# Optimization experiments

Measured on AMD Instinct MI355X. Metric: run time of the kernel, lower is better.

## Reference

```python
import jax, jax.numpy as jnp
import numpy as np

T, B, IN, H1, H2, OUT = 1024, 512, 20, 128, 64, 3

def _uniform(key, shape, bound):
    return jax.random.uniform(key, shape, jnp.float32, -bound, bound)

def setup_inputs() -> dict:
    key = jax.random.key(0)
    ks = jax.random.split(key, 11)
    b1 = 1.0 / np.sqrt(H1)
    b2 = 1.0 / np.sqrt(H2)
    return {
        "x": jax.random.normal(ks[0], (T, B, IN), jnp.float32),
        "W_ih0": _uniform(ks[1], (4 * H1, IN), b1),
        "W_hh0": _uniform(ks[2], (4 * H1, H1), b1),
        "b_ih0": _uniform(ks[3], (4 * H1,), b1),
        "b_hh0": _uniform(ks[4], (4 * H1,), b1),
        "W_ih1": _uniform(ks[5], (4 * H2, H1), b2),
        "W_hh1": _uniform(ks[6], (4 * H2, H2), b2),
        "b_ih1": _uniform(ks[7], (4 * H2,), b2),
        "b_hh1": _uniform(ks[8], (4 * H2,), b2),
        "W_d": _uniform(ks[9], (OUT, H2), b2),
        "b_d": _uniform(ks[10], (OUT,), b2),
    }

def _lstm_layer(x, W_ih, W_hh, b_ih, b_hh, hidden):
    # x: (T, B, in_dim); PyTorch gate order: i, f, g, o
    batch = x.shape[1]
    x_proj = jnp.einsum("tbi,gi->tbg", x, W_ih) + (b_ih + b_hh)  # (T,B,4H)

    def step(carry, xp):
        h, c = carry
        gates = xp + h @ W_hh.T  # (B,4H)
        i, f, g, o = jnp.split(gates, 4, axis=-1)
        i = jax.nn.sigmoid(i)
        f = jax.nn.sigmoid(f)
        g = jnp.tanh(g)
        o = jax.nn.sigmoid(o)
        c = f * c + i * g
        h = o * jnp.tanh(c)
        return (h, c), h

    h0 = jnp.zeros((batch, hidden), x.dtype)
    c0 = jnp.zeros((batch, hidden), x.dtype)
    _, ys = jax.lax.scan(step, (h0, c0), x_proj)
    return ys  # (T, B, H)

def reference(x, W_ih0, W_hh0, b_ih0, b_hh0, W_ih1, W_hh1, b_ih1, b_hh1, W_d, b_d):
    h1 = _lstm_layer(x, W_ih0, W_hh0, b_ih0, b_hh0, H1)   # (T,B,128)
    h2 = _lstm_layer(h1, W_ih1, W_hh1, b_ih1, b_hh1, H2)  # (T,B,64)
    # Faithful to original: lstm_out[:, -1, :] in seq-first layout picks the
    # last batch element at every timestep -> (T, 64)
    last = h2[:, -1, :]
    act = jax.nn.relu(last)
    # Dropout in eval mode is identity.
    return act @ W_d.T + b_d  # (T, 3)
```

## Files before the change

kernel.cpp:

```cpp
#include <hip/hip_runtime.h>
#include <hip/hip_bf16.h>


#define T_STEPS 1024
#define BATCH   512
#define IN_F    20
#define H1_     128
#define H2_     64
#define OUT_F   3
#define G1_     (4*H1_)
#define G2_     (4*H2_)

typedef float f4 __attribute__((ext_vector_type(4)));
typedef unsigned int u32;
typedef u32 u4 __attribute__((ext_vector_type(4)));
typedef _Float16 h2 __attribute__((ext_vector_type(2)));

__device__ __forceinline__ float sigmoidf_(float x) {
    return 1.0f / (1.0f + __expf(-x));
}
__device__ __forceinline__ float tanhf_(float x) {
    return 1.0f - 2.0f / (__expf(2.0f * x) + 1.0f);
}
__device__ __forceinline__ h2 as_h2(u32 v) {
    union { u32 u; h2 h; } c; c.u = v; return c.h;
}
__device__ __forceinline__ u32 pkh(float a, float b) {
    union { _Float16 h[2]; u32 u; } c;
    c.h[0] = (_Float16)a; c.h[1] = (_Float16)b; return c.u;
}
__device__ __forceinline__ float fdot2_(h2 a, h2 b, float c) {
#if __has_builtin(__builtin_amdgcn_fdot2)
    return __builtin_amdgcn_fdot2(a, b, c, false);
#else
    float d = c;
    asm("v_dot2_f32_f16 %0, %1, %2, %0" : "+v"(d) : "v"(a), "v"(b));
    return d;
#endif
}

__global__ void xproj_kernel(const float* __restrict__ x,
                             const float* __restrict__ W_ih0,
                             const float* __restrict__ b_ih0,
                             const float* __restrict__ b_hh0,
                             float* __restrict__ xp1)
{
    const int t = blockIdx.x;
    const int g = threadIdx.x;
    const float* xr = x + ((size_t)t * BATCH + (BATCH - 1)) * IN_F;
    const float* w  = W_ih0 + g * IN_F;
    float acc = b_ih0[g] + b_hh0[g];
#pragma unroll
    for (int i = 0; i < IN_F; ++i) acc = fmaf(xr[i], w[i], acc);
    xp1[t * G1_ + g] = acc;
}

__global__ __attribute__((amdgpu_flat_work_group_size(512, 512),
                          amdgpu_waves_per_eu(2, 2)))
void lstm1_kernel(const float* __restrict__ xp1,
                  const float* __restrict__ W_hh0,
                  float* __restrict__ h1seq)
{
    const int tid = threadIdx.x;

    __shared__ u4    swW[512 * 17];
    __shared__ u4    shhi[16];
    __shared__ u4    shlo[16];
    __shared__ float sg[G1_];

    {
        const float* wr = W_hh0 + (size_t)tid * H1_;
#pragma unroll
        for (int j = 0; j < 16; ++j) {
            const f4 lo = *(const f4*)(wr + j * 8);
            const f4 hi = *(const f4*)(wr + j * 8 + 4);
            u4 pk;
            pk.x = pkh(lo.x, lo.y);
            pk.y = pkh(lo.z, lo.w);
            pk.z = pkh(hi.x, hi.y);
            pk.w = pkh(hi.z, hi.w);
            swW[tid * 17 + j] = pk;
        }
    }
    if (tid < 16) { shhi[tid] = u4{0,0,0,0}; shlo[tid] = u4{0,0,0,0}; }
    float c1 = 0.0f;
    __syncthreads();

    const u4* wrow = swW + tid * 17;
    float xp_cur = xp1[tid];

    for (int t = 0; t < T_STEPS; ++t) {
        float xp_next;
        {
            const int tn = (t + 1 < T_STEPS) ? (t + 1) : (T_STEPS - 1);
            xp_next = xp1[(size_t)tn * G1_ + tid];
        }

        float a0 = 0.f, a1 = 0.f, a2 = 0.f, a3 = 0.f;
#pragma unroll
        for (int j = 0; j < 16; ++j) {
            const u4 wq = wrow[j];
            const u4 hh = shhi[j];
            const u4 hl = shlo[j];
            a0 = fdot2_(as_h2(wq.x), as_h2(hh.x), a0);
            a1 = fdot2_(as_h2(wq.y), as_h2(hh.y), a1);
            a0 = fdot2_(as_h2(wq.z), as_h2(hh.z), a0);
            a1 = fdot2_(as_h2(wq.w), as_h2(hh.w), a1);
            a2 = fdot2_(as_h2(wq.x), as_h2(hl.x), a2);
            a3 = fdot2_(as_h2(wq.y), as_h2(hl.y), a3);
            a2 = fdot2_(as_h2(wq.z), as_h2(hl.z), a2);
            a3 = fdot2_(as_h2(wq.w), as_h2(hl.w), a3);
        }
        sg[tid] = ((a0 + a1) + 0.000244140625f * (a2 + a3)) + xp_cur;
        __syncthreads();

        if (tid < H1_) {
            const float vi = sg[tid];
            const float vf = sg[H1_ + tid];
            const float vg = sg[2 * H1_ + tid];
            const float vo = sg[3 * H1_ + tid];
            c1 = fmaf(sigmoidf_(vf), c1, sigmoidf_(vi) * tanhf_(vg));
            const float h = sigmoidf_(vo) * tanhf_(c1);
            const _Float16 hh16 = (_Float16)h;
            const float hrem = (h - (float)hh16) * 4096.0f;
            ((_Float16*)shhi)[tid] = hh16;
            ((_Float16*)shlo)[tid] = (_Float16)hrem;
            h1seq[(size_t)t * H1_ + tid] = h;
        }
        __syncthreads();
        xp_cur = xp_next;
    }
}

__global__ void xproj2_kernel(const float* __restrict__ h1seq,
                              const float* __restrict__ W_ih1,
                              const float* __restrict__ b_ih1,
                              const float* __restrict__ b_hh1,
                              float* __restrict__ xp2)
{
    const int t = blockIdx.x;
    const int g = threadIdx.x;
    __shared__ f4 sh[H1_ / 4];
    if (g < H1_ / 4) sh[g] = ((const f4*)(h1seq + (size_t)t * H1_))[g];
    __syncthreads();
    const f4* w = (const f4*)(W_ih1 + (size_t)g * H1_);
    float ax = 0.f, ay = 0.f, az = 0.f, aw = 0.f;
#pragma unroll
    for (int k = 0; k < H1_ / 4; ++k) {
        const f4 h4 = sh[k]; const f4 w4 = w[k];
        ax = fmaf(w4.x, h4.x, ax); ay = fmaf(w4.y, h4.y, ay);
        az = fmaf(w4.z, h4.z, az); aw = fmaf(w4.w, h4.w, aw);
    }
    xp2[(size_t)t * G2_ + g] = ((ax + ay) + (az + aw)) + b_ih1[g] + b_hh1[g];
}

__global__ __attribute__((amdgpu_flat_work_group_size(256, 256),
                          amdgpu_waves_per_eu(1, 1)))
void lstm2_kernel(const float* __restrict__ xp2,
                  const float* __restrict__ W_hh1,
                  float* __restrict__ h2seq)
{
    const int tid = threadIdx.x;

    __shared__ u4    swW2[256 * 9];
    __shared__ u4    shhi[8];
    __shared__ u4    shlo[8];
    __shared__ float sg2[G2_];

    {
        const float* wr = W_hh1 + (size_t)tid * H2_;
#pragma unroll
        for (int j = 0; j < 8; ++j) {
            const f4 lo = *(const f4*)(wr + j * 8);
            const f4 hi = *(const f4*)(wr + j * 8 + 4);
            u4 pk;
            pk.x = pkh(lo.x, lo.y);
            pk.y = pkh(lo.z, lo.w);
            pk.z = pkh(hi.x, hi.y);
            pk.w = pkh(hi.z, hi.w);
            swW2[tid * 9 + j] = pk;
        }
    }
    if (tid < 8) { shhi[tid] = u4{0,0,0,0}; shlo[tid] = u4{0,0,0,0}; }
    float c2 = 0.0f;
    __syncthreads();

    const u4* wrow = swW2 + tid * 9;
    float xp_cur = xp2[tid];

    for (int t = 0; t < T_STEPS; ++t) {
        float xp_next;
        {
            const int tn = (t + 1 < T_STEPS) ? (t + 1) : (T_STEPS - 1);
            xp_next = xp2[(size_t)tn * G2_ + tid];
        }

        float a0 = 0.f, a1 = 0.f, a2 = 0.f, a3 = 0.f;
#pragma unroll
        for (int j = 0; j < 8; ++j) {
            const u4 wq = wrow[j];
            const u4 hh = shhi[j];
            const u4 hl = shlo[j];
            a0 = fdot2_(as_h2(wq.x), as_h2(hh.x), a0);
            a1 = fdot2_(as_h2(wq.y), as_h2(hh.y), a1);
            a0 = fdot2_(as_h2(wq.z), as_h2(hh.z), a0);
            a1 = fdot2_(as_h2(wq.w), as_h2(hh.w), a1);
            a2 = fdot2_(as_h2(wq.x), as_h2(hl.x), a2);
            a3 = fdot2_(as_h2(wq.y), as_h2(hl.y), a3);
            a2 = fdot2_(as_h2(wq.z), as_h2(hl.z), a2);
            a3 = fdot2_(as_h2(wq.w), as_h2(hl.w), a3);
        }
        sg2[tid] = ((a0 + a1) + 0.000244140625f * (a2 + a3)) + xp_cur;
        __syncthreads();

        if (tid < H2_) {
            const float vi = sg2[tid];
            const float vf = sg2[H2_ + tid];
            const float vg = sg2[2 * H2_ + tid];
            const float vo = sg2[3 * H2_ + tid];
            c2 = fmaf(sigmoidf_(vf), c2, sigmoidf_(vi) * tanhf_(vg));
            const float h = sigmoidf_(vo) * tanhf_(c2);
            const _Float16 hh16 = (_Float16)h;
            const float hrem = (h - (float)hh16) * 4096.0f;
            ((_Float16*)shhi)[tid] = hh16;
            ((_Float16*)shlo)[tid] = (_Float16)hrem;
            h2seq[(size_t)t * H2_ + tid] = h;
        }
        __syncthreads();
        xp_cur = xp_next;
    }
}

__global__ void head_kernel(const float* __restrict__ h2seq,
                            const float* __restrict__ W_d,
                            const float* __restrict__ b_d,
                            float* __restrict__ out)
{
    const int idx = blockIdx.x * blockDim.x + threadIdx.x;
    if (idx >= T_STEPS * OUT_F) return;
    const int t = idx / OUT_F;
    const int o = idx - t * OUT_F;
    const float* hr = h2seq + (size_t)t * H2_;
    const float* w  = W_d + o * H2_;
    float acc = b_d[o];
#pragma unroll
    for (int j = 0; j < H2_; ++j) acc = fmaf(fmaxf(hr[j], 0.0f), w[j], acc);
    out[idx] = acc;
}

extern "C" void kernel_launch(void* const* d_in, const int* in_sizes, int n_in,
                              void* d_out, int out_size, void* d_ws, size_t ws_size,
                              hipStream_t stream) {
    const float* x     = (const float*)d_in[0];
    const float* W_ih0 = (const float*)d_in[1];
    const float* W_hh0 = (const float*)d_in[2];
    const float* b_ih0 = (const float*)d_in[3];
    const float* b_hh0 = (const float*)d_in[4];
    const float* W_ih1 = (const float*)d_in[5];
    const float* W_hh1 = (const float*)d_in[6];
    const float* b_ih1 = (const float*)d_in[7];
    const float* b_hh1 = (const float*)d_in[8];
    const float* W_d   = (const float*)d_in[9];
    const float* b_d   = (const float*)d_in[10];

    float* out   = (float*)d_out;
    float* xp1   = (float*)d_ws;
    float* h1seq = xp1 + (size_t)T_STEPS * G1_;
    float* h2seq = h1seq + (size_t)T_STEPS * H1_;
    float* xp2   = xp1;

    hipLaunchKernelGGL(xproj_kernel, dim3(T_STEPS), dim3(G1_), 0, stream,
                       x, W_ih0, b_ih0, b_hh0, xp1);
    hipLaunchKernelGGL(lstm1_kernel, dim3(1), dim3(512), 0, stream,
                       xp1, W_hh0, h1seq);
    hipLaunchKernelGGL(xproj2_kernel, dim3(T_STEPS), dim3(G2_), 0, stream,
                       h1seq, W_ih1, b_ih1, b_hh1, xp2);
    hipLaunchKernelGGL(lstm2_kernel, dim3(1), dim3(256), 0, stream,
                       xp2, W_hh1, h2seq);
    hipLaunchKernelGGL(head_kernel, dim3((T_STEPS * OUT_F + 255) / 256), dim3(256),
                       0, stream, h2seq, W_d, b_d, out);
}
```

Baseline: 1.962 ms.

## Split LSTM recurrent dot products across twice the threads with split-K reduction

```diff
diff --git a/kernel.cpp b/kernel.cpp
--- a/kernel.cpp
+++ b/kernel.cpp
@@ -14,7 +14,7 @@
 typedef float f4 __attribute__((ext_vector_type(4)));
 typedef unsigned int u32;
 typedef u32 u4 __attribute__((ext_vector_type(4)));
-typedef _Float16 h2 __attribute__((ext_vector_type(2)));
+typedef _Float16 h2t __attribute__((ext_vector_type(2)));
 
 __device__ __forceinline__ float sigmoidf_(float x) {
     return 1.0f / (1.0f + __expf(-x));
@@ -22,14 +22,14 @@
 __device__ __forceinline__ float tanhf_(float x) {
     return 1.0f - 2.0f / (__expf(2.0f * x) + 1.0f);
 }
-__device__ __forceinline__ h2 as_h2(u32 v) {
-    union { u32 u; h2 h; } c; c.u = v; return c.h;
+__device__ __forceinline__ h2t as_h2(u32 v) {
+    union { u32 u; h2t h; } c; c.u = v; return c.h;
 }
 __device__ __forceinline__ u32 pkh(float a, float b) {
     union { _Float16 h[2]; u32 u; } c;
     c.h[0] = (_Float16)a; c.h[1] = (_Float16)b; return c.u;
 }
-__device__ __forceinline__ float fdot2_(h2 a, h2 b, float c) {
+__device__ __forceinline__ float fdot2_(h2t a, h2t b, float c) {
 #if __has_builtin(__builtin_amdgcn_fdot2)
     return __builtin_amdgcn_fdot2(a, b, c, false);
 #else
@@ -38,6 +38,27 @@
     return d;
 #endif
 }
+__device__ __forceinline__ u4 packq(const float* p) {
+    const f4 a = *(const f4*)p;
+    const f4 b = *(const f4*)(p + 4);
+    u4 pk;
+    pk.x = pkh(a.x, a.y); pk.y = pkh(a.z, a.w);
+    pk.z = pkh(b.x, b.y); pk.w = pkh(b.z, b.w);
+    return pk;
+}
+
+#define LO_SCALE_INV 0.000244140625f
+
+#define DOTQ(WQ, HH, HL)                                                      \
+    { const u4 hh_ = (HH); const u4 hl_ = (HL);                               \
+      a0 = fdot2_(as_h2((WQ).x), as_h2(hh_.x), a0);                           \
+      a1 = fdot2_(as_h2((WQ).y), as_h2(hh_.y), a1);                           \
+      a0 = fdot2_(as_h2((WQ).z), as_h2(hh_.z), a0);                           \
+      a1 = fdot2_(as_h2((WQ).w), as_h2(hh_.w), a1);                           \
+      a2 = fdot2_(as_h2((WQ).x), as_h2(hl_.x), a2);                           \
+      a3 = fdot2_(as_h2((WQ).y), as_h2(hl_.y), a3);                           \
+      a2 = fdot2_(as_h2((WQ).z), as_h2(hl_.z), a2);                           \
+      a3 = fdot2_(as_h2((WQ).w), as_h2(hl_.w), a3); }
 
 __global__ void xproj_kernel(const float* __restrict__ x,
                              const float* __restrict__ W_ih0,
@@ -55,70 +76,80 @@
     xp1[t * G1_ + g] = acc;
 }
 
-__global__ __attribute__((amdgpu_flat_work_group_size(512, 512),
-                          amdgpu_waves_per_eu(2, 2)))
+__global__ void pack_kernel(const float* __restrict__ W_hh0,
+                            const float* __restrict__ W_hh1,
+                            u4* __restrict__ wpk1,
+                            u4* __restrict__ wpk2)
+{
+    const int idx = blockIdx.x * blockDim.x + threadIdx.x;
+    if (idx < 4096) {
+        const int r = idx >> 2, qq = idx & 3;
+        const int g = r & 511, hf = r >> 9;
+        wpk1[r * 4 + qq] = packq(W_hh0 + (size_t)g * H1_ + hf * 64 + 32 + 8 * qq);
+    } else if (idx < 4096 + 1024) {
+        const int i2 = idx - 4096;
+        const int r2 = i2 >> 1, qq = i2 & 1;
+        const int g2 = r2 & 255, hf = r2 >> 8;
+        wpk2[r2 * 2 + qq] = packq(W_hh1 + (size_t)g2 * H2_ + hf * 32 + 16 + 8 * qq);
+    }
+}
+
+__global__ __attribute__((amdgpu_flat_work_group_size(1024, 1024),
+                          amdgpu_waves_per_eu(4, 4)))
 void lstm1_kernel(const float* __restrict__ xp1,
                   const float* __restrict__ W_hh0,
+                  const u4* __restrict__ wpk1,
                   float* __restrict__ h1seq)
 {
     const int tid = threadIdx.x;
-
-    __shared__ u4    swW[512 * 17];
+    const int g   = tid & 511;
+    const int hf  = tid >> 9;
+    const int r   = hf * 512 + g;
+
+    __shared__ u4    swW[1024 * 5];
     __shared__ u4    shhi[16];
     __shared__ u4    shlo[16];
-    __shared__ float sg[G1_];
+    __shared__ float sp1[1024];
 
     {
-        const float* wr = W_hh0 + (size_t)tid * H1_;
-#pragma unroll
-        for (int j = 0; j < 16; ++j) {
-            const f4 lo = *(const f4*)(wr + j * 8);
-            const f4 hi = *(const f4*)(wr + j * 8 + 4);
-            u4 pk;
-            pk.x = pkh(lo.x, lo.y);
-            pk.y = pkh(lo.z, lo.w);
-            pk.z = pkh(hi.x, hi.y);
-            pk.w = pkh(hi.z, hi.w);
-            swW[tid * 17 + j] = pk;
-        }
+        const float* wr = W_hh0 + (size_t)g * H1_ + hf * 64;
+#pragma unroll
+        for (int q = 0; q < 4; ++q) swW[r * 5 + q] = packq(wr + q * 8);
     }
     if (tid < 16) { shhi[tid] = u4{0,0,0,0}; shlo[tid] = u4{0,0,0,0}; }
     float c1 = 0.0f;
     __syncthreads();
 
-    const u4* wrow = swW + tid * 17;
-    float xp_cur = xp1[tid];
+    const u4* wk = wpk1 + (size_t)r * 4;
+    float xp_cur = (hf == 0) ? xp1[g] : 0.0f;
 
     for (int t = 0; t < T_STEPS; ++t) {
-        float xp_next;
-        {
+        float xp_next = 0.0f;
+        if (hf == 0) {
             const int tn = (t + 1 < T_STEPS) ? (t + 1) : (T_STEPS - 1);
-            xp_next = xp1[(size_t)tn * G1_ + tid];
-        }
+            xp_next = xp1[(size_t)tn * G1_ + g];
+        }
+        const u4 w4_ = wk[0], w5_ = wk[1], w6_ = wk[2], w7_ = wk[3];
 
         float a0 = 0.f, a1 = 0.f, a2 = 0.f, a3 = 0.f;
 #pragma unroll
-        for (int j = 0; j < 16; ++j) {
-            const u4 wq = wrow[j];
-            const u4 hh = shhi[j];
-            const u4 hl = shlo[j];
-            a0 = fdot2_(as_h2(wq.x), as_h2(hh.x), a0);
-            a1 = fdot2_(as_h2(wq.y), as_h2(hh.y), a1);
-            a0 = fdot2_(as_h2(wq.z), as_h2(hh.z), a0);
-            a1 = fdot2_(as_h2(wq.w), as_h2(hh.w), a1);
-            a2 = fdot2_(as_h2(wq.x), as_h2(hl.x), a2);
-            a3 = fdot2_(as_h2(wq.y), as_h2(hl.y), a3);
-            a2 = fdot2_(as_h2(wq.z), as_h2(hl.z), a2);
-            a3 = fdot2_(as_h2(wq.w), as_h2(hl.w), a3);
-        }
-        sg[tid] = ((a0 + a1) + 0.000244140625f * (a2 + a3)) + xp_cur;
+        for (int q = 0; q < 4; ++q) {
+            const u4 wq = swW[r * 5 + q];
+            DOTQ(wq, shhi[hf * 8 + q], shlo[hf * 8 + q]);
+        }
+        DOTQ(w4_, shhi[hf * 8 + 4], shlo[hf * 8 + 4]);
+        DOTQ(w5_, shhi[hf * 8 + 5], shlo[hf * 8 + 5]);
+        DOTQ(w6_, shhi[hf * 8 + 6], shlo[hf * 8 + 6]);
+        DOTQ(w7_, shhi[hf * 8 + 7], shlo[hf * 8 + 7]);
+
+        sp1[g * 2 + hf] = ((a0 + a1) + LO_SCALE_INV * (a2 + a3)) + xp_cur;
         __syncthreads();
 
         if (tid < H1_) {
-            const float vi = sg[tid];
-            const float vf = sg[H1_ + tid];
-            const float vg = sg[2 * H1_ + tid];
-            const float vo = sg[3 * H1_ + tid];
+            const float vi = sp1[tid * 2]              + sp1[tid * 2 + 1];
+            const float vf = sp1[(H1_ + tid) * 2]      + sp1[(H1_ + tid) * 2 + 1];
+            const float vg = sp1[(2 * H1_ + tid) * 2]  + sp1[(2 * H1_ + tid) * 2 + 1];
+            const float vo = sp1[(3 * H1_ + tid) * 2]  + sp1[(3 * H1_ + tid) * 2 + 1];
             c1 = fmaf(sigmoidf_(vf), c1, sigmoidf_(vi) * tanhf_(vg));
             const float h = sigmoidf_(vo) * tanhf_(c1);
             const _Float16 hh16 = (_Float16)h;
@@ -154,70 +185,61 @@
     xp2[(size_t)t * G2_ + g] = ((ax + ay) + (az + aw)) + b_ih1[g] + b_hh1[g];
 }
 
-__global__ __attribute__((amdgpu_flat_work_group_size(256, 256),
-                          amdgpu_waves_per_eu(1, 1)))
+__global__ __attribute__((amdgpu_flat_work_group_size(512, 512),
+                          amdgpu_waves_per_eu(2, 2)))
 void lstm2_kernel(const float* __restrict__ xp2,
                   const float* __restrict__ W_hh1,
+                  const u4* __restrict__ wpk2,
                   float* __restrict__ h2seq)
 {
     const int tid = threadIdx.x;
-
-    __shared__ u4    swW2[256 * 9];
+    const int g2  = tid & 255;
+    const int hf  = tid >> 8;
+    const int r2  = hf * 256 + g2;
+
+    __shared__ u4    swW2[512 * 3];
     __shared__ u4    shhi[8];
     __shared__ u4    shlo[8];
-    __shared__ float sg2[G2_];
+    __shared__ float sp2[512];
 
     {
-        const float* wr = W_hh1 + (size_t)tid * H2_;
-#pragma unroll
-        for (int j = 0; j < 8; ++j) {
-            const f4 lo = *(const f4*)(wr + j * 8);
-            const f4 hi = *(const f4*)(wr + j * 8 + 4);
-            u4 pk;
-            pk.x = pkh(lo.x, lo.y);
-            pk.y = pkh(lo.z, lo.w);
-            pk.z = pkh(hi.x, hi.y);
-            pk.w = pkh(hi.z, hi.w);
-            swW2[tid * 9 + j] = pk;
-        }
+        const float* wr = W_hh1 + (size_t)g2 * H2_ + hf * 32;
+        swW2[r2 * 3 + 0] = packq(wr);
+        swW2[r2 * 3 + 1] = packq(wr + 8);
     }
     if (tid < 8) { shhi[tid] = u4{0,0,0,0}; shlo[tid] = u4{0,0,0,0}; }
     float c2 = 0.0f;
     __syncthreads();
 
-    const u4* wrow = swW2 + tid * 9;
-    float xp_cur = xp2[tid];
+    const u4* wk = wpk2 + (size_t)r2 * 2;
+    float xp_cur = (hf == 0) ? xp2[g2] : 0.0f;
 
     for (int t = 0; t < T_STEPS; ++t) {
-        float xp_next;
+        float xp_next = 0.0f;
+        if (hf == 0) {
+            const int tn = (t + 1 < T_STEPS) ? (t + 1) : (T_STEPS - 1);
+            xp_next = xp2[(size_t)tn * G2_ + g2];
+        }
+        const u4 w2_ = wk[0], w3_ = wk[1];
+
+        float a0 = 0.f, a1 = 0.f, a2 = 0.f, a3 = 0.f;
         {
-            const int tn = (t + 1 < T_STEPS) ? (t + 1) : (T_STEPS - 1);
-            xp_next = xp2[(size_t)tn * G2_ + tid];
-        }
-
-        float a0 = 0.f, a1 = 0.f, a2 = 0.f, a3 = 0.f;
-#pragma unroll
-        for (int j = 0; j < 8; ++j) {
-            const u4 wq = wrow[j];
-            const u4 hh = shhi[j];
-            const u4 hl = shlo[j];
-            a0 = fdot2_(as_h2(wq.x), as_h2(hh.x), a0);
-            a1 = fdot2_(as_h2(wq.y), as_h2(hh.y), a1);
-            a0 = fdot2_(as_h2(wq.z), as_h2(hh.z), a0);
-            a1 = fdot2_(as_h2(wq.w), as_h2(hh.w), a1);
-            a2 = fdot2_(as_h2(wq.x), as_h2(hl.x), a2);
-            a3 = fdot2_(as_h2(wq.y), as_h2(hl.y), a3);
-            a2 = fdot2_(as_h2(wq.z), as_h2(hl.z), a2);
-            a3 = fdot2_(as_h2(wq.w), as_h2(hl.w), a3);
-        }
-        sg2[tid] = ((a0 + a1) + 0.000244140625f * (a2 + a3)) + xp_cur;
+            const u4 wq0 = swW2[r2 * 3 + 0];
+            DOTQ(wq0, shhi[hf * 4 + 0], shlo[hf * 4 + 0]);
+            const u4 wq1 = swW2[r2 * 3 + 1];
+            DOTQ(wq1, shhi[hf * 4 + 1], shlo[hf * 4 + 1]);
+        }
+        DOTQ(w2_, shhi[hf * 4 + 2], shlo[hf * 4 + 2]);
+        DOTQ(w3_, shhi[hf * 4 + 3], shlo[hf * 4 + 3]);
+
+        sp2[g2 * 2 + hf] = ((a0 + a1) + LO_SCALE_INV * (a2 + a3)) + xp_cur;
         __syncthreads();
 
         if (tid < H2_) {
-            const float vi = sg2[tid];
-            const float vf = sg2[H2_ + tid];
-            const float vg = sg2[2 * H2_ + tid];
-            const float vo = sg2[3 * H2_ + tid];
+            const float vi = sp2[tid * 2]              + sp2[tid * 2 + 1];
+            const float vf = sp2[(H2_ + tid) * 2]      + sp2[(H2_ + tid) * 2 + 1];
+            const float vg = sp2[(2 * H2_ + tid) * 2]  + sp2[(2 * H2_ + tid) * 2 + 1];
+            const float vo = sp2[(3 * H2_ + tid) * 2]  + sp2[(3 * H2_ + tid) * 2 + 1];
             c2 = fmaf(sigmoidf_(vf), c2, sigmoidf_(vi) * tanhf_(vg));
             const float h = sigmoidf_(vo) * tanhf_(c2);
             const _Float16 hh16 = (_Float16)h;
@@ -267,16 +289,20 @@
     float* xp1   = (float*)d_ws;
     float* h1seq = xp1 + (size_t)T_STEPS * G1_;
     float* h2seq = h1seq + (size_t)T_STEPS * H1_;
+    u4*    wpk1  = (u4*)(h2seq + (size_t)T_STEPS * H2_);
+    u4*    wpk2  = wpk1 + 1024 * 4;
     float* xp2   = xp1;
 
     hipLaunchKernelGGL(xproj_kernel, dim3(T_STEPS), dim3(G1_), 0, stream,
                        x, W_ih0, b_ih0, b_hh0, xp1);
-    hipLaunchKernelGGL(lstm1_kernel, dim3(1), dim3(512), 0, stream,
-                       xp1, W_hh0, h1seq);
+    hipLaunchKernelGGL(pack_kernel, dim3(20), dim3(256), 0, stream,
+                       W_hh0, W_hh1, wpk1, wpk2);
+    hipLaunchKernelGGL(lstm1_kernel, dim3(1), dim3(1024), 0, stream,
+                       xp1, W_hh0, wpk1, h1seq);
     hipLaunchKernelGGL(xproj2_kernel, dim3(T_STEPS), dim3(G2_), 0, stream,
                        h1seq, W_ih1, b_ih1, b_hh1, xp2);
-    hipLaunchKernelGGL(lstm2_kernel, dim3(1), dim3(256), 0, stream,
-                       xp2, W_hh1, h2seq);
+    hipLaunchKernelGGL(lstm2_kernel, dim3(1), dim3(512), 0, stream,
+                       xp2, W_hh1, wpk2, h2seq);
     hipLaunchKernelGGL(head_kernel, dim3((T_STEPS * OUT_F + 255) / 256), dim3(256),
                        0, stream, h2seq, W_d, b_d, out);
 }
```

After: 1.675 ms. -14.6%, faster.
